# Optimization experiments

Hardware: AMD Instinct MI355X
Metric: run time of the kernel (lower is better)

## Reference

```python
import jax, jax.numpy as jnp
import numpy as np

DELTA_V = 0.5
DELTA_D = 1.5
ALPHA = 1.0
BETA = 1.0
GAMMA = 0.001
K = 64  # max number of instance ids per batch element


def _safe_sqrt(sq):
    # sqrt with zero-safe gradient: exact where sq > 0, returns 0 otherwise
    pos = sq > 0
    return jnp.sqrt(jnp.where(pos, sq, 1.0)) * pos.astype(sq.dtype)


def setup_inputs() -> dict:
    key = jax.random.key(0)
    k1, k2 = jax.random.split(key)
    B, N, D = 16, 65536, 32
    embeddings = jax.random.normal(k1, (B, N, D), dtype=jnp.float32)
    instance_ids = jax.random.randint(k2, (B, N), 0, K, dtype=jnp.int32)
    mask = jnp.ones((B, N), dtype=bool)
    return {"embeddings": embeddings, "instance_ids": instance_ids, "mask": mask}


def reference(embeddings, instance_ids, mask):
    B, N, D = embeddings.shape
    f32 = embeddings.dtype
    valid = mask & (instance_ids >= 0)
    # flat segment id per point; invalid points go to dump segment B*K
    batch_off = jnp.arange(B, dtype=jnp.int32)[:, None] * K
    seg = jnp.where(valid, batch_off + instance_ids, B * K).reshape(-1)
    w = valid.reshape(-1).astype(f32)
    flat = embeddings.reshape(-1, D)

    # per-instance sums / counts -> means  (segment reduce, memory-bound)
    sums = jax.ops.segment_sum(flat * w[:, None], seg, num_segments=B * K + 1)[: B * K]
    counts = jax.ops.segment_sum(w, seg, num_segments=B * K + 1)[: B * K]
    means_flat = sums / jnp.maximum(counts, 1.0)[:, None]  # (B*K, D)
    present = (counts > 0).reshape(B, K)                   # (B, K)
    num_inst = present.sum(-1).astype(f32)                 # (B,)
    valid_b = (num_inst >= 2).astype(f32)                  # batches counted as samples

    # ---- variance (pull) loss ----
    seg_clip = jnp.minimum(seg, B * K - 1)
    diff = flat - means_flat[seg_clip]                     # (B*N, D)
    dist = _safe_sqrt((diff * diff).sum(-1))
    pen = jnp.maximum(dist - DELTA_V, 0.0) ** 2 * w
    inst_pen = jax.ops.segment_sum(pen, seg, num_segments=B * K + 1)[: B * K]
    inst_pen = (inst_pen / jnp.maximum(counts, 1.0)).reshape(B, K)
    var_b = (inst_pen * present).sum(-1) / jnp.maximum(num_inst, 1.0)

    # ---- distance (push) loss: pairwise over instance means ----
    means = means_flat.reshape(B, K, D)
    dsq = ((means[:, :, None, :] - means[:, None, :, :]) ** 2).sum(-1)  # (B, K, K)
    iu = jnp.arange(K)
    pair_m = present[:, :, None] & present[:, None, :] & (iu[:, None] < iu[None, :])
    pair_mf = pair_m.astype(f32)
    pdist = _safe_sqrt(jnp.where(pair_m, dsq, 1.0)) * pair_mf
    pen2 = jnp.maximum(2.0 * DELTA_D - pdist, 0.0) ** 2 * pair_mf
    num_pairs = num_inst * (num_inst - 1.0) / 2.0
    dist_b = pen2.sum((1, 2)) / jnp.maximum(num_pairs, 1.0)

    # ---- regularization loss ----
    mnorm = _safe_sqrt((means * means).sum(-1)) * present.astype(f32)  # (B, K)
    reg_b = mnorm.sum(-1) / jnp.maximum(num_inst, 1.0)

    denom = jnp.maximum(valid_b.sum(), 1.0)
    var_loss = (var_b * valid_b).sum() / denom
    dist_loss = (dist_b * valid_b).sum() / denom
    reg_loss = (reg_b * valid_b).sum() / denom
    total = ALPHA * var_loss + BETA * dist_loss + GAMMA * reg_loss
    return jnp.stack([total, var_loss, dist_loss, reg_loss])
```

## Files before the change

kernel.cpp:

```cpp
#include <hip/hip_runtime.h>
#include <cstdint>

#define BB 16
#define NN 65536
#define DD 32
#define KK 64
#define DELTA_V 0.5f
#define DELTA_D 1.5f

typedef short bf16x8 __attribute__((ext_vector_type(8)));
typedef float f32x16 __attribute__((ext_vector_type(16)));

__device__ __forceinline__ short f2bf(float x) {
    union { float f; unsigned u; } v; v.f = x;
    const unsigned r = v.u + 0x7FFFu + ((v.u >> 16) & 1u);
    return (short)(r >> 16);
}

__device__ __forceinline__ void gll16(const float* g, float* l) {
    __builtin_amdgcn_global_load_lds(
        (const __attribute__((address_space(1))) unsigned int*)g,
        (__attribute__((address_space(3))) unsigned int*)l, 16, 0, 0);
}

#define K1_BLOCKS 2048
#define K1_PPB 512

__global__ __launch_bounds__(64) void k_accum(
    const float* __restrict__ emb, const int* __restrict__ ids,
    const int* __restrict__ mask, float* __restrict__ parts,
    float* __restrict__ pcnt)
{
    __shared__ float ebuf[32][32];
    const int lane = threadIdx.x;
    const int half = lane >> 5, d32 = lane & 31;
    const int blk  = blockIdx.x;
    const int b    = blk >> 7;
    const size_t p0 = (size_t)b * NN + (size_t)(blk & 127) * K1_PPB;

    f32x16 acc0 = {}, acc1 = {};
    int c0 = 0, c1 = 0;
    const int m0 = d32, m1 = d32 + 32;

    for (int s = 0; s < K1_PPB / 64; ++s) {
        const size_t ps = p0 + s * 64;
        const int idr = ids[ps + lane];
        const int mkr = mask[ps + lane];
        const int vid = (mkr != 0 && (unsigned)idr < KK) ? idr : -1;
#pragma unroll
        for (int h = 0; h < 2; ++h) {
            const float* gsrc = emb + (ps + h * 32) * DD;
#pragma unroll
            for (int i = 0; i < 4; ++i)
                gll16(gsrc + i * 256 + lane * 4, &ebuf[0][0] + i * 256);
            asm volatile("s_waitcnt vmcnt(0)" ::: "memory");
            __builtin_amdgcn_sched_barrier(0);
#pragma unroll
            for (int q = 0; q < 2; ++q) {
                bf16x8 bfB, a0, a1;
#pragma unroll
                for (int e = 0; e < 8; ++e) {
                    const int pt = q * 16 + 8 * half + e;
                    bfB[e] = f2bf(ebuf[pt][d32]);
                    const int s_lo = __builtin_amdgcn_readlane(vid, h * 32 + q * 16 + e);
                    const int s_hi = __builtin_amdgcn_readlane(vid, h * 32 + q * 16 + 8 + e);
                    const int sel  = half ? s_hi : s_lo;
                    const bool h0 = (sel == m0), h1 = (sel == m1);
                    a0[e] = h0 ? (short)0x3F80 : (short)0;
                    a1[e] = h1 ? (short)0x3F80 : (short)0;
                    c0 += h0 ? 1 : 0;
                    c1 += h1 ? 1 : 0;
                }
                acc0 = __builtin_amdgcn_mfma_f32_32x32x16_bf16(a0, bfB, acc0, 0, 0, 0);
                acc1 = __builtin_amdgcn_mfma_f32_32x32x16_bf16(a1, bfB, acc1, 0, 0, 0);
            }
        }
    }

    float* pb = parts + (size_t)blk * (KK * DD);
#pragma unroll
    for (int r = 0; r < 16; ++r) {
        const int mrow = (r & 3) + 8 * (r >> 2) + 4 * half;
        pb[mrow * DD + d32]        = acc0[r];
        pb[(32 + mrow) * DD + d32] = acc1[r];
    }
    c0 += __shfl_down(c0, 32);
    c1 += __shfl_down(c1, 32);
    if (lane < 32) {
        pcnt[(size_t)blk * KK + lane]      = (float)c0;
        pcnt[(size_t)blk * KK + 32 + lane] = (float)c1;
    }
}

__global__ __launch_bounds__(128) void k_reduce(
    const float* __restrict__ parts, const float* __restrict__ pcnt,
    float* __restrict__ mu)
{
    const int b = blockIdx.x >> 4;
    const int c = blockIdx.x & 15;
    const int tid = threadIdx.x;
    __shared__ float t4[128][4];
    __shared__ float scnt[4];

    const float* pc = pcnt + (size_t)b * 128 * KK + c * 4;
#pragma unroll
    for (int u = 0; u < 4; ++u) t4[tid][u] = pc[(size_t)tid * KK + u];
    __syncthreads();
    if (tid < 4) {
        float s = 0.f;
        for (int j = 0; j < 128; ++j) s += t4[j][tid];
        scnt[tid] = s;
    }
    __syncthreads();

    const int e = c * 128 + tid;
    const float* pp = parts + (size_t)b * 128 * (KK * DD) + e;
    float s = 0.f;
    for (int j = 0; j < 128; ++j) s += pp[(size_t)j * (KK * DD)];
    const int k = e >> 5, d = e & 31;
    const float cnt = scnt[tid >> 5];
    mu[(size_t)b * KK * 33 + k * 33 + d] = s / fmaxf(cnt, 1.f);
    if (tid < 4) mu[(size_t)b * KK * 33 + (c * 4 + tid) * 33 + 32] = scnt[tid];
}

#define K2_BPB 64
#define K2_PTS (NN / K2_BPB)

__global__ __launch_bounds__(256) void k_pull(
    const float* __restrict__ emb, const int* __restrict__ ids,
    const int* __restrict__ mask, const float* __restrict__ mu,
    float* __restrict__ varacc)
{
    __shared__ float smu[KK * 33];
    __shared__ float red[4];
    const int tid = threadIdx.x;
    const int b   = blockIdx.x >> 6;
    const int blk = blockIdx.x & 63;

    const float* mub = mu + (size_t)b * KK * 33;
    for (int i = tid; i < KK * 33; i += 256) smu[i] = mub[i];
    __syncthreads();

    const size_t p0 = (size_t)b * NN + (size_t)blk * K2_PTS;
    float accv = 0.f;
    for (int p = tid; p < K2_PTS; p += 256) {
        const int id = ids[p0 + p];
        const bool v = (mask[p0 + p] != 0) && ((unsigned)id < KK);
        const int sid = v ? id : 0;
        const float* mr = smu + sid * 33;
        const float4* e = (const float4*)(emb + (p0 + p) * DD);
        float dsq = 0.f;
#pragma unroll
        for (int q = 0; q < 8; ++q) {
            const float4 t = e[q];
            float a;
            a = t.x - mr[4 * q + 0]; dsq = fmaf(a, a, dsq);
            a = t.y - mr[4 * q + 1]; dsq = fmaf(a, a, dsq);
            a = t.z - mr[4 * q + 2]; dsq = fmaf(a, a, dsq);
            a = t.w - mr[4 * q + 3]; dsq = fmaf(a, a, dsq);
        }
        const float dist = (dsq > 0.f) ? sqrtf(dsq) : 0.f;
        float pen = fmaxf(dist - DELTA_V, 0.f);
        pen = pen * pen;
        if (v) accv += pen / fmaxf(mr[32], 1.f);
    }
    for (int off = 32; off; off >>= 1) accv += __shfl_down(accv, off);
    if ((tid & 63) == 0) red[tid >> 6] = accv;
    __syncthreads();
    if (tid == 0) atomicAdd(&varacc[b], red[0] + red[1] + red[2] + red[3]);
}

__global__ __launch_bounds__(256) void k_push_reg(
    const float* __restrict__ mu, float* __restrict__ regb,
    float* __restrict__ distb)
{
    const int b = blockIdx.x;
    const int tid = threadIdx.x;
    __shared__ float lm[KK][DD + 1];
    __shared__ float lcnt[KK];
    __shared__ float red[4];

    const float* mub = mu + (size_t)b * KK * 33;
    for (int i = tid; i < KK * DD; i += 256) {
        const int k = i >> 5, d = i & 31;
        lm[k][d] = mub[k * 33 + d];
    }
    if (tid < KK) lcnt[tid] = mub[tid * 33 + 32];
    __syncthreads();

    float ninst = 0.f;
    if (tid < KK) {
        const float c = lcnt[tid];
        const float pres = (c > 0.f) ? 1.f : 0.f;
        float sq = 0.f;
#pragma unroll
        for (int d = 0; d < DD; ++d) { const float m = lm[tid][d]; sq = fmaf(m, m, sq); }
        float nm = ((sq > 0.f) ? sqrtf(sq) : 0.f) * pres;
        float pn = pres;
        for (int off = 32; off; off >>= 1) {
            pn += __shfl_down(pn, off);
            nm += __shfl_down(nm, off);
        }
        if (tid == 0) {
            ninst = pn;
            regb[b] = nm / fmaxf(pn, 1.f);
        }
    }

    float acc = 0.f;
    for (int idx = tid; idx < KK * KK; idx += 256) {
        const int i = idx >> 6, j = idx & 63;
        if (i < j && lcnt[i] > 0.f && lcnt[j] > 0.f) {
            float dsq = 0.f;
#pragma unroll
            for (int d = 0; d < DD; ++d) {
                const float df = lm[i][d] - lm[j][d];
                dsq = fmaf(df, df, dsq);
            }
            const float pd = (dsq > 0.f) ? sqrtf(dsq) : 0.f;
            const float pen = fmaxf(2.f * DELTA_D - pd, 0.f);
            acc = fmaf(pen, pen, acc);
        }
    }
    for (int off = 32; off; off >>= 1) acc += __shfl_down(acc, off);
    if ((tid & 63) == 0) red[tid >> 6] = acc;
    __syncthreads();
    if (tid == 0) {
        const float tot = red[0] + red[1] + red[2] + red[3];
        const float np = ninst * (ninst - 1.f) * 0.5f;
        distb[b] = tot / fmaxf(np, 1.f);
    }
}

__global__ __launch_bounds__(64) void k_final(
    const float* __restrict__ mu, const float* __restrict__ varacc,
    const float* __restrict__ regb, const float* __restrict__ distb,
    float* __restrict__ out)
{
    const int tid = threadIdx.x;
    __shared__ float s_var[BB], s_valid[BB];
    if (tid < BB) {
        const int b = tid;
        float ni = 0.f;
        for (int k = 0; k < KK; ++k)
            ni += (mu[(size_t)b * KK * 33 + k * 33 + 32] > 0.f) ? 1.f : 0.f;
        s_var[tid]   = varacc[b] / fmaxf(ni, 1.f);
        s_valid[tid] = (ni >= 2.f) ? 1.f : 0.f;
    }
    __syncthreads();
    if (tid == 0) {
        float denom = 0.f, v = 0.f, d = 0.f, r = 0.f;
        for (int b = 0; b < BB; ++b) {
            const float vb = s_valid[b];
            denom += vb;
            v += s_var[b] * vb;
            d += distb[b] * vb;
            r += regb[b] * vb;
        }
        denom = fmaxf(denom, 1.f);
        v /= denom; d /= denom; r /= denom;
        out[0] = v + d + 0.001f * r;
        out[1] = v;
        out[2] = d;
        out[3] = r;
    }
}

extern "C" void kernel_launch(void* const* d_in, const int* in_sizes, int n_in,
                              void* d_out, int out_size, void* d_ws, size_t ws_size,
                              hipStream_t stream)
{
    const float* emb  = (const float*)d_in[0];
    const int*   ids  = (const int*)d_in[1];
    const int*   mask = (const int*)d_in[2];

    float* ws     = (float*)d_ws;
    float* parts  = ws;
    float* pcnt   = parts + (size_t)K1_BLOCKS * KK * DD;
    float* mu     = pcnt + (size_t)K1_BLOCKS * KK;
    float* varacc = mu + (size_t)BB * KK * 33;
    float* regb   = varacc + BB;
    float* distb  = regb + BB;

    hipMemsetAsync(varacc, 0, BB * sizeof(float), stream);

    k_accum<<<K1_BLOCKS, 64, 0, stream>>>(emb, ids, mask, parts, pcnt);
    k_reduce<<<BB * 16, 128, 0, stream>>>(parts, pcnt, mu);
    k_pull<<<BB * K2_BPB, 256, 0, stream>>>(emb, ids, mask, mu, varacc);
    k_push_reg<<<BB, 256, 0, stream>>>(mu, regb, distb);
    k_final<<<1, 64, 0, stream>>>(mu, varacc, regb, distb, (float*)d_out);
}
```

Before: 94.35 us.

## Restructure accumulation into 4-wave blocks and fuse reduce with push/reg kernel

The accumulation kernel moves from 64-thread blocks to 256-thread blocks with four waves. Each wave loads its points with direct float4 register loads into a padded LDS tile, instead of global_load_lds. The four wave partials are summed in LDS before being written, which cuts the partials buffer from 2048 to 1024 slabs. The separate reduce and push/reg kernels are merged into one per-batch kernel, and the pull kernel writes per-block partials instead of using atomics, which removes the memset. The cost is that the fused reduce now runs on only 16 blocks, so cross-block parallelism for the partial reduction drops.

```diff
diff --git a/kernel.cpp b/kernel.cpp
--- a/kernel.cpp
+++ b/kernel.cpp
@@ -17,110 +17,161 @@
     return (short)(r >> 16);
 }
 
-__device__ __forceinline__ void gll16(const float* g, float* l) {
-    __builtin_amdgcn_global_load_lds(
-        (const __attribute__((address_space(1))) unsigned int*)g,
-        (__attribute__((address_space(3))) unsigned int*)l, 16, 0, 0);
-}
-
-#define K1_BLOCKS 2048
-#define K1_PPB 512
-
-__global__ __launch_bounds__(64) void k_accum(
+#define K1_BPB 64
+#define K1_PPB 1024
+#define K1_WPTS 256
+
+__global__ __launch_bounds__(256, 4) void k_accum(
     const float* __restrict__ emb, const int* __restrict__ ids,
     const int* __restrict__ mask, float* __restrict__ parts,
     float* __restrict__ pcnt)
 {
-    __shared__ float ebuf[32][32];
-    const int lane = threadIdx.x;
+    __shared__ float tb[4][64][33];
+    __shared__ float lc2[4][KK];
+    const int tid  = threadIdx.x;
+    const int w    = tid >> 6, lane = tid & 63;
     const int half = lane >> 5, d32 = lane & 31;
-    const int blk  = blockIdx.x;
-    const int b    = blk >> 7;
-    const size_t p0 = (size_t)b * NN + (size_t)(blk & 127) * K1_PPB;
+    const int b    = blockIdx.x >> 6;
+    const int blk  = blockIdx.x & 63;
+    const size_t pw = (size_t)b * NN + (size_t)blk * K1_PPB + (size_t)w * K1_WPTS;
 
     f32x16 acc0 = {}, acc1 = {};
     int c0 = 0, c1 = 0;
     const int m0 = d32, m1 = d32 + 32;
-
-    for (int s = 0; s < K1_PPB / 64; ++s) {
-        const size_t ps = p0 + s * 64;
+    float (*T)[33] = tb[w];
+
+    for (int s = 0; s < 4; ++s) {
+        const size_t ps = pw + s * 64;
+        const float4* ep = (const float4*)(emb + (ps + lane) * DD);
+        float4 r[8];
+#pragma unroll
+        for (int q = 0; q < 8; ++q) r[q] = ep[q];
         const int idr = ids[ps + lane];
         const int mkr = mask[ps + lane];
         const int vid = (mkr != 0 && (unsigned)idr < KK) ? idr : -1;
-#pragma unroll
-        for (int h = 0; h < 2; ++h) {
-            const float* gsrc = emb + (ps + h * 32) * DD;
-#pragma unroll
-            for (int i = 0; i < 4; ++i)
-                gll16(gsrc + i * 256 + lane * 4, &ebuf[0][0] + i * 256);
-            asm volatile("s_waitcnt vmcnt(0)" ::: "memory");
-            __builtin_amdgcn_sched_barrier(0);
-#pragma unroll
-            for (int q = 0; q < 2; ++q) {
-                bf16x8 bfB, a0, a1;
-#pragma unroll
-                for (int e = 0; e < 8; ++e) {
-                    const int pt = q * 16 + 8 * half + e;
-                    bfB[e] = f2bf(ebuf[pt][d32]);
-                    const int s_lo = __builtin_amdgcn_readlane(vid, h * 32 + q * 16 + e);
-                    const int s_hi = __builtin_amdgcn_readlane(vid, h * 32 + q * 16 + 8 + e);
-                    const int sel  = half ? s_hi : s_lo;
-                    const bool h0 = (sel == m0), h1 = (sel == m1);
-                    a0[e] = h0 ? (short)0x3F80 : (short)0;
-                    a1[e] = h1 ? (short)0x3F80 : (short)0;
-                    c0 += h0 ? 1 : 0;
-                    c1 += h1 ? 1 : 0;
-                }
-                acc0 = __builtin_amdgcn_mfma_f32_32x32x16_bf16(a0, bfB, acc0, 0, 0, 0);
-                acc1 = __builtin_amdgcn_mfma_f32_32x32x16_bf16(a1, bfB, acc1, 0, 0, 0);
+
+        float* myrow = T[lane];
+#pragma unroll
+        for (int q = 0; q < 8; ++q) {
+            myrow[4 * q + 0] = r[q].x; myrow[4 * q + 1] = r[q].y;
+            myrow[4 * q + 2] = r[q].z; myrow[4 * q + 3] = r[q].w;
+        }
+
+#pragma unroll
+        for (int q = 0; q < 4; ++q) {
+            bf16x8 bfB, a0, a1;
+#pragma unroll
+            for (int e = 0; e < 8; ++e) {
+                bfB[e] = f2bf(T[q * 16 + 8 * half + e][d32]);
+                const int s_lo = __builtin_amdgcn_readlane(vid, q * 16 + e);
+                const int s_hi = __builtin_amdgcn_readlane(vid, q * 16 + 8 + e);
+                const int sel  = half ? s_hi : s_lo;
+                const bool h0 = (sel == m0), h1 = (sel == m1);
+                a0[e] = h0 ? (short)0x3F80 : (short)0;
+                a1[e] = h1 ? (short)0x3F80 : (short)0;
+                c0 += h0 ? 1 : 0;
+                c1 += h1 ? 1 : 0;
             }
-        }
-    }
-
-    float* pb = parts + (size_t)blk * (KK * DD);
+            acc0 = __builtin_amdgcn_mfma_f32_32x32x16_bf16(a0, bfB, acc0, 0, 0, 0);
+            acc1 = __builtin_amdgcn_mfma_f32_32x32x16_bf16(a1, bfB, acc1, 0, 0, 0);
+        }
+    }
+    __syncthreads();
+
 #pragma unroll
     for (int r = 0; r < 16; ++r) {
         const int mrow = (r & 3) + 8 * (r >> 2) + 4 * half;
-        pb[mrow * DD + d32]        = acc0[r];
-        pb[(32 + mrow) * DD + d32] = acc1[r];
+        T[mrow][d32]      = acc0[r];
+        T[32 + mrow][d32] = acc1[r];
     }
     c0 += __shfl_down(c0, 32);
     c1 += __shfl_down(c1, 32);
-    if (lane < 32) {
-        pcnt[(size_t)blk * KK + lane]      = (float)c0;
-        pcnt[(size_t)blk * KK + 32 + lane] = (float)c1;
-    }
-}
-
-__global__ __launch_bounds__(128) void k_reduce(
+    if (lane < 32) { lc2[w][lane] = (float)c0; lc2[w][lane + 32] = (float)c1; }
+    __syncthreads();
+
+    float* pb = parts + (size_t)blockIdx.x * (KK * DD);
+    for (int i = tid; i < KK * DD; i += 256) {
+        const int row = i >> 5, col = i & 31;
+        pb[i] = tb[0][row][col] + tb[1][row][col] + tb[2][row][col] + tb[3][row][col];
+    }
+    if (tid < KK)
+        pcnt[(size_t)blockIdx.x * KK + tid] =
+            lc2[0][tid] + lc2[1][tid] + lc2[2][tid] + lc2[3][tid];
+}
+
+__global__ __launch_bounds__(256) void k_reduce_push(
     const float* __restrict__ parts, const float* __restrict__ pcnt,
-    float* __restrict__ mu)
-{
-    const int b = blockIdx.x >> 4;
-    const int c = blockIdx.x & 15;
+    float* __restrict__ mu, float* __restrict__ regb,
+    float* __restrict__ distb)
+{
+    const int b = blockIdx.x;
     const int tid = threadIdx.x;
-    __shared__ float t4[128][4];
-    __shared__ float scnt[4];
-
-    const float* pc = pcnt + (size_t)b * 128 * KK + c * 4;
-#pragma unroll
-    for (int u = 0; u < 4; ++u) t4[tid][u] = pc[(size_t)tid * KK + u];
-    __syncthreads();
-    if (tid < 4) {
+    __shared__ float lm[KK][DD + 1];
+    __shared__ float lcnt[KK];
+    __shared__ float red[4];
+
+    if (tid < KK) {
         float s = 0.f;
-        for (int j = 0; j < 128; ++j) s += t4[j][tid];
-        scnt[tid] = s;
-    }
-    __syncthreads();
-
-    const int e = c * 128 + tid;
-    const float* pp = parts + (size_t)b * 128 * (KK * DD) + e;
-    float s = 0.f;
-    for (int j = 0; j < 128; ++j) s += pp[(size_t)j * (KK * DD)];
-    const int k = e >> 5, d = e & 31;
-    const float cnt = scnt[tid >> 5];
-    mu[(size_t)b * KK * 33 + k * 33 + d] = s / fmaxf(cnt, 1.f);
-    if (tid < 4) mu[(size_t)b * KK * 33 + (c * 4 + tid) * 33 + 32] = scnt[tid];
+        for (int j = 0; j < K1_BPB; ++j)
+            s += pcnt[((size_t)b * K1_BPB + j) * KK + tid];
+        lcnt[tid] = s;
+        mu[(size_t)b * KK * 33 + tid * 33 + 32] = s;
+    }
+    __syncthreads();
+
+    for (int e = tid; e < KK * DD; e += 256) {
+        float s = 0.f;
+        for (int j = 0; j < K1_BPB; ++j)
+            s += parts[((size_t)b * K1_BPB + j) * (KK * DD) + e];
+        const int k = e >> 5, d = e & 31;
+        const float m = s / fmaxf(lcnt[k], 1.f);
+        lm[k][d] = m;
+        mu[(size_t)b * KK * 33 + k * 33 + d] = m;
+    }
+    __syncthreads();
+
+    float ninst = 0.f;
+    if (tid < KK) {
+        const float c = lcnt[tid];
+        const float pres = (c > 0.f) ? 1.f : 0.f;
+        float sq = 0.f;
+#pragma unroll
+        for (int d = 0; d < DD; ++d) { const float m = lm[tid][d]; sq = fmaf(m, m, sq); }
+        float nm = ((sq > 0.f) ? sqrtf(sq) : 0.f) * pres;
+        float pn = pres;
+        for (int off = 32; off; off >>= 1) {
+            pn += __shfl_down(pn, off);
+            nm += __shfl_down(nm, off);
+        }
+        if (tid == 0) {
+            ninst = pn;
+            regb[b] = nm / fmaxf(pn, 1.f);
+        }
+    }
+
+    float acc = 0.f;
+    for (int idx = tid; idx < KK * KK; idx += 256) {
+        const int i = idx >> 6, j = idx & 63;
+        if (i < j && lcnt[i] > 0.f && lcnt[j] > 0.f) {
+            float dsq = 0.f;
+#pragma unroll
+            for (int d = 0; d < DD; ++d) {
+                const float df = lm[i][d] - lm[j][d];
+                dsq = fmaf(df, df, dsq);
+            }
+            const float pd = (dsq > 0.f) ? sqrtf(dsq) : 0.f;
+            const float pen = fmaxf(2.f * DELTA_D - pd, 0.f);
+            acc = fmaf(pen, pen, acc);
+        }
+    }
+    for (int off = 32; off; off >>= 1) acc += __shfl_down(acc, off);
+    if ((tid & 63) == 0) red[tid >> 6] = acc;
+    __syncthreads();
+    if (tid == 0) {
+        const float tot = red[0] + red[1] + red[2] + red[3];
+        const float np = ninst * (ninst - 1.f) * 0.5f;
+        distb[b] = tot / fmaxf(np, 1.f);
+    }
 }
 
 #define K2_BPB 64
@@ -129,7 +180,7 @@
 __global__ __launch_bounds__(256) void k_pull(
     const float* __restrict__ emb, const int* __restrict__ ids,
     const int* __restrict__ mask, const float* __restrict__ mu,
-    float* __restrict__ varacc)
+    float* __restrict__ varpart)
 {
     __shared__ float smu[KK * 33];
     __shared__ float red[4];
@@ -167,73 +218,12 @@
     for (int off = 32; off; off >>= 1) accv += __shfl_down(accv, off);
     if ((tid & 63) == 0) red[tid >> 6] = accv;
     __syncthreads();
-    if (tid == 0) atomicAdd(&varacc[b], red[0] + red[1] + red[2] + red[3]);
-}
-
-__global__ __launch_bounds__(256) void k_push_reg(
-    const float* __restrict__ mu, float* __restrict__ regb,
-    float* __restrict__ distb)
-{
-    const int b = blockIdx.x;
-    const int tid = threadIdx.x;
-    __shared__ float lm[KK][DD + 1];
-    __shared__ float lcnt[KK];
-    __shared__ float red[4];
-
-    const float* mub = mu + (size_t)b * KK * 33;
-    for (int i = tid; i < KK * DD; i += 256) {
-        const int k = i >> 5, d = i & 31;
-        lm[k][d] = mub[k * 33 + d];
-    }
-    if (tid < KK) lcnt[tid] = mub[tid * 33 + 32];
-    __syncthreads();
-
-    float ninst = 0.f;
-    if (tid < KK) {
-        const float c = lcnt[tid];
-        const float pres = (c > 0.f) ? 1.f : 0.f;
-        float sq = 0.f;
-#pragma unroll
-        for (int d = 0; d < DD; ++d) { const float m = lm[tid][d]; sq = fmaf(m, m, sq); }
-        float nm = ((sq > 0.f) ? sqrtf(sq) : 0.f) * pres;
-        float pn = pres;
-        for (int off = 32; off; off >>= 1) {
-            pn += __shfl_down(pn, off);
-            nm += __shfl_down(nm, off);
-        }
-        if (tid == 0) {
-            ninst = pn;
-            regb[b] = nm / fmaxf(pn, 1.f);
-        }
-    }
-
-    float acc = 0.f;
-    for (int idx = tid; idx < KK * KK; idx += 256) {
-        const int i = idx >> 6, j = idx & 63;
-        if (i < j && lcnt[i] > 0.f && lcnt[j] > 0.f) {
-            float dsq = 0.f;
-#pragma unroll
-            for (int d = 0; d < DD; ++d) {
-                const float df = lm[i][d] - lm[j][d];
-                dsq = fmaf(df, df, dsq);
-            }
-            const float pd = (dsq > 0.f) ? sqrtf(dsq) : 0.f;
-            const float pen = fmaxf(2.f * DELTA_D - pd, 0.f);
-            acc = fmaf(pen, pen, acc);
-        }
-    }
-    for (int off = 32; off; off >>= 1) acc += __shfl_down(acc, off);
-    if ((tid & 63) == 0) red[tid >> 6] = acc;
-    __syncthreads();
-    if (tid == 0) {
-        const float tot = red[0] + red[1] + red[2] + red[3];
-        const float np = ninst * (ninst - 1.f) * 0.5f;
-        distb[b] = tot / fmaxf(np, 1.f);
-    }
+    if (tid == 0)
+        varpart[blockIdx.x] = red[0] + red[1] + red[2] + red[3];
 }
 
 __global__ __launch_bounds__(64) void k_final(
-    const float* __restrict__ mu, const float* __restrict__ varacc,
+    const float* __restrict__ mu, const float* __restrict__ varpart,
     const float* __restrict__ regb, const float* __restrict__ distb,
     float* __restrict__ out)
 {
@@ -244,7 +234,9 @@
         float ni = 0.f;
         for (int k = 0; k < KK; ++k)
             ni += (mu[(size_t)b * KK * 33 + k * 33 + 32] > 0.f) ? 1.f : 0.f;
-        s_var[tid]   = varacc[b] / fmaxf(ni, 1.f);
+        float vs = 0.f;
+        for (int j = 0; j < K2_BPB; ++j) vs += varpart[b * K2_BPB + j];
+        s_var[tid]   = vs / fmaxf(ni, 1.f);
         s_valid[tid] = (ni >= 2.f) ? 1.f : 0.f;
     }
     __syncthreads();
@@ -274,19 +266,16 @@
     const int*   ids  = (const int*)d_in[1];
     const int*   mask = (const int*)d_in[2];
 
-    float* ws     = (float*)d_ws;
-    float* parts  = ws;
-    float* pcnt   = parts + (size_t)K1_BLOCKS * KK * DD;
-    float* mu     = pcnt + (size_t)K1_BLOCKS * KK;
-    float* varacc = mu + (size_t)BB * KK * 33;
-    float* regb   = varacc + BB;
-    float* distb  = regb + BB;
-
-    hipMemsetAsync(varacc, 0, BB * sizeof(float), stream);
-
-    k_accum<<<K1_BLOCKS, 64, 0, stream>>>(emb, ids, mask, parts, pcnt);
-    k_reduce<<<BB * 16, 128, 0, stream>>>(parts, pcnt, mu);
-    k_pull<<<BB * K2_BPB, 256, 0, stream>>>(emb, ids, mask, mu, varacc);
-    k_push_reg<<<BB, 256, 0, stream>>>(mu, regb, distb);
-    k_final<<<1, 64, 0, stream>>>(mu, varacc, regb, distb, (float*)d_out);
-}
+    float* ws      = (float*)d_ws;
+    float* parts   = ws;
+    float* pcnt    = parts + (size_t)BB * K1_BPB * KK * DD;
+    float* mu      = pcnt + (size_t)BB * K1_BPB * KK;
+    float* varpart = mu + (size_t)BB * KK * 33;
+    float* regb    = varpart + BB * K2_BPB;
+    float* distb   = regb + BB;
+
+    k_accum<<<BB * K1_BPB, 256, 0, stream>>>(emb, ids, mask, parts, pcnt);
+    k_reduce_push<<<BB, 256, 0, stream>>>(parts, pcnt, mu, regb, distb);
+    k_pull<<<BB * K2_BPB, 256, 0, stream>>>(emb, ids, mask, mu, varpart);
+    k_final<<<1, 64, 0, stream>>>(mu, varpart, regb, distb, (float*)d_out);
+}
```

After: 100.9 us. +7.0%, slower.
